# Kernel optimization log

Hardware: AMD Instinct MI355X
Metric: run time of the kernel (lower is better)

## Reference

```python
import jax, jax.numpy as jnp
import numpy as np
import math

NUM_PAGES = 256   # total KV pool pages
PAGE_SIZE = 16    # tokens per page
N_USED = 128      # pages in this sequence -> kv_len = 2048
H = 32            # num_heads
D = 128           # head_dim
LQ = 2048         # query length (== kv_len, causal prefill)


def setup_inputs() -> dict:
    key = jax.random.key(0)
    k_q, k_k, k_v, k_ks, k_vs = jax.random.split(key, 5)
    q = jax.random.normal(k_q, (1, H, LQ, D), dtype=jnp.float32)
    K_pages = jax.random.randint(k_k, (NUM_PAGES, PAGE_SIZE, H, D), -128, 128, dtype=jnp.int8)
    V_pages = jax.random.randint(k_v, (NUM_PAGES, PAGE_SIZE, H, D), -128, 128, dtype=jnp.int8)
    K_scale = jax.random.uniform(k_ks, (NUM_PAGES, 1, H, 1), dtype=jnp.float16, minval=0.001, maxval=0.02)
    V_scale = jax.random.uniform(k_vs, (NUM_PAGES, 1, H, 1), dtype=jnp.float16, minval=0.001, maxval=0.02)
    pages = jnp.arange(N_USED, dtype=jnp.int32)  # page table for this sequence
    return {"q": q, "K_pages": K_pages, "V_pages": V_pages,
            "K_scale": K_scale, "V_scale": V_scale, "pages": pages}


def _gather_dequant(pages_i8, scales, page_ids):
    # pages_i8: [P, ps, H, D] int8; scales: [P, 1, H, 1] fp16; page_ids: [n]
    x = pages_i8[page_ids].astype(jnp.float32) * scales[page_ids].astype(jnp.float32)
    n, ps, h, d = x.shape
    # cat along tokens, then [S,H,D] -> [1,H,S,D]
    return jnp.transpose(x.reshape(n * ps, h, d), (1, 0, 2))[None]


def reference(q, K_pages, V_pages, K_scale, V_scale, pages):
    K = _gather_dequant(K_pages, K_scale, pages)  # [1,H,S,D]
    V = _gather_dequant(V_pages, V_scale, pages)  # [1,H,S,D]
    lq = q.shape[2]
    s = K.shape[2]
    scale = 1.0 / math.sqrt(q.shape[-1])
    scores = jnp.einsum('bhqd,bhkd->bhqk', q, K) * scale  # [1,H,LQ,S]
    # torch is_causal: top-left aligned causal mask (j <= i)
    causal = jnp.tril(jnp.ones((lq, s), dtype=bool))
    scores = jnp.where(causal[None, None], scores, -jnp.inf)
    attn = jax.nn.softmax(scores, axis=-1)
    return jnp.einsum('bhqk,bhkd->bhqd', attn, V)
```

## Files before the change

### kernel.cpp

```cpp
#include <hip/hip_runtime.h>
#include <stdint.h>

#define NHEADS 32
#define DHEAD  128
#define LQ     2048
#define PAGE   16
#define QTILE  64
#define NQT    32
#define KVB    32
#define KPAD   136

typedef _Float16 f16x8 __attribute__((ext_vector_type(8)));
typedef _Float16 f16x2v __attribute__((ext_vector_type(2)));
typedef float    f32x4 __attribute__((ext_vector_type(4)));

__global__ __launch_bounds__(256, 2)
void paged_attn_kernel(const float* __restrict__ q,
                       const int*   __restrict__ Kp,
                       const int*   __restrict__ Vp,
                       const float* __restrict__ Kscale,
                       const float* __restrict__ Vscale,
                       const int*   __restrict__ pages,
                       float* __restrict__ out)
{
    __shared__ _Float16 Ks[KVB][KPAD];
    __shared__ __align__(16) _Float16 Vt[DHEAD][KVB];

    const int tid  = threadIdx.x;
    const int w    = tid >> 6;
    const int lane = tid & 63;
    const int g    = lane >> 4;
    const int c    = lane & 15;

    const int bx = blockIdx.x;
    const int h  = bx & (NHEADS - 1);
    const int p  = bx >> 5;
    const int qa = p, qb = NQT - 1 - p;
    const int q0a = qa * QTILE, q0b = qb * QTILE;

    const float qscale = 0.08838834764831845f * 1.44269504088896340736f;

    f16x8 qfa[4], qfb[4];
    {
        const float* qpa = q + ((size_t)h * LQ + q0a + w * 16 + c) * DHEAD;
        const float* qpb = q + ((size_t)h * LQ + q0b + w * 16 + c) * DHEAD;
        #pragma unroll
        for (int t = 0; t < 4; ++t)
            #pragma unroll
            for (int i = 0; i < 8; ++i) {
                qfa[t][i] = (_Float16)(qpa[t * 32 + g * 8 + i] * qscale);
                qfb[t][i] = (_Float16)(qpb[t * 32 + g * 8 + i] * qscale);
            }
    }

    f32x4 oaccA[8], oaccB[8];
    #pragma unroll
    for (int d = 0; d < 8; ++d) { oaccA[d] = (f32x4){0,0,0,0}; oaccB[d] = (f32x4){0,0,0,0}; }
    float mA = -1e30f, lA = 0.f, mB = -1e30f, lB = 0.f;

    const int ntiles = 2 * qb + 2;
    const int skv = tid >> 3;
    const int sa  = tid & 7;
    char* vtb = (char*)&Vt[0][0];

    auto issue = [&](int tile, int4* krD, int4* vrD, float& ksD, float& vsD) {
        const int t_glob = tile * KVB + skv;
        const int pg  = pages[t_glob >> 4];
        const int tok = t_glob & 15;
        const size_t base = (((size_t)pg * PAGE + tok) * NHEADS + h) * DHEAD + sa * 16;
        const int4* kp4 = (const int4*)(Kp + base);
        const int4* vp4 = (const int4*)(Vp + base);
        #pragma unroll
        for (int j = 0; j < 4; ++j) { krD[j] = kp4[j]; vrD[j] = vp4[j]; }
        ksD = Kscale[pg * NHEADS + h];
        vsD = Vscale[pg * NHEADS + h];
    };

    auto compute = [&](int kv0, const f16x8 (*kf)[4], const f16x8* qf, int q0t,
                       f32x4* oacc, float& mr, float& lr) {
        f32x4 s0 = (f32x4){0,0,0,0}, s1 = (f32x4){0,0,0,0};
        #pragma unroll
        for (int t = 0; t < 4; ++t) {
            s0 = __builtin_amdgcn_mfma_f32_16x16x32_f16(kf[0][t], qf[t], s0, 0, 0, 0);
            s1 = __builtin_amdgcn_mfma_f32_16x16x32_f16(kf[1][t], qf[t], s1, 0, 0, 0);
        }
        const int dq = (q0t + w * 16 + c) - (kv0 + 4 * g);
        #pragma unroll
        for (int r = 0; r < 4; ++r) {
            if (r > dq)      s0[r] = -1e30f;
            if (r > dq - 16) s1[r] = -1e30f;
        }
        float tm = fmaxf(fmaxf(fmaxf(s0[0], s0[1]), fmaxf(s0[2], s0[3])),
                         fmaxf(fmaxf(s1[0], s1[1]), fmaxf(s1[2], s1[3])));
        tm = fmaxf(tm, __shfl_xor(tm, 16, 64));
        tm = fmaxf(tm, __shfl_xor(tm, 32, 64));
        const float mn    = fmaxf(mr, tm);
        const float alpha = exp2f(mr - mn);
        mr = mn;
        float p0[4], p1[4];
        #pragma unroll
        for (int r = 0; r < 4; ++r) {
            p0[r] = exp2f(s0[r] - mn);
            p1[r] = exp2f(s1[r] - mn);
        }
        float rs = ((p0[0] + p0[1]) + (p0[2] + p0[3])) +
                   ((p1[0] + p1[1]) + (p1[2] + p1[3]));
        rs += __shfl_xor(rs, 16, 64);
        rs += __shfl_xor(rs, 32, 64);
        lr = lr * alpha + rs;
        float aR[4];
        #pragma unroll
        for (int r = 0; r < 4; ++r) aR[r] = __shfl(alpha, 20 * g + r, 64);
        #pragma unroll
        for (int d = 0; d < 8; ++d)
            #pragma unroll
            for (int r = 0; r < 4; ++r)
                oacc[d][r] *= aR[r];
        f16x2v t0, t1, t2, t3;
        t0[0] = (_Float16)p0[0]; t0[1] = (_Float16)p0[1];
        t1[0] = (_Float16)p0[2]; t1[1] = (_Float16)p0[3];
        t2[0] = (_Float16)p1[0]; t2[1] = (_Float16)p1[1];
        t3[0] = (_Float16)p1[2]; t3[1] = (_Float16)p1[3];
        const int w00 = __builtin_bit_cast(int, t0);
        const int w01 = __builtin_bit_cast(int, t1);
        const int w10 = __builtin_bit_cast(int, t2);
        const int w11 = __builtin_bit_cast(int, t3);
        const int srcL = ((g & 1) << 5) | c;
        const int srcH = srcL + 16;
        const int e0A = __shfl(w00, srcL, 64), e0B = __shfl(w10, srcL, 64);
        const int e1A = __shfl(w01, srcL, 64), e1B = __shfl(w11, srcL, 64);
        const int e2A = __shfl(w00, srcH, 64), e2B = __shfl(w10, srcH, 64);
        const int e3A = __shfl(w01, srcH, 64), e3B = __shfl(w11, srcH, 64);
        const bool hi = g >= 2;
        uint4 aw;
        aw.x = (unsigned)(hi ? e0B : e0A);
        aw.y = (unsigned)(hi ? e1B : e1A);
        aw.z = (unsigned)(hi ? e2B : e2A);
        aw.w = (unsigned)(hi ? e3B : e3A);
        const f16x8 pa = __builtin_bit_cast(f16x8, aw);
        #pragma unroll
        for (int d = 0; d < 8; ++d) {
            const int dcol = d * 16 + c;
            unsigned off = (unsigned)(dcol * (KVB * 2) + g * 16);
            off ^= (unsigned)(((dcol >> 3) & 7) << 4);
            f16x8 vf = *(const f16x8*)(vtb + off);
            oacc[d] = __builtin_amdgcn_mfma_f32_16x16x32_f16(pa, vf, oacc[d], 0, 0, 0);
        }
    };

    int4 krA[4], vrA[4]; float ksrA = 0.f, vsrA = 0.f;
    int4 krB[4], vrB[4]; float ksrB = 0.f, vsrB = 0.f;
    issue(0, krA, vrA, ksrA, vsrA);

    for (int tile = 0; tile < ntiles; ++tile) {
        const int kv0 = tile * KVB;

        {
            const int* ki = (const int*)krA;
            const int* vi = (const int*)vrA;
            f16x8 klo, khi;
            #pragma unroll
            for (int i = 0; i < 8; ++i) {
                klo[i] = (_Float16)((float)ki[i]     * ksrA);
                khi[i] = (_Float16)((float)ki[8 + i] * ksrA);
            }
            *(f16x8*)&Ks[skv][sa * 16]     = klo;
            *(f16x8*)&Ks[skv][sa * 16 + 8] = khi;
            #pragma unroll
            for (int j = 0; j < 16; ++j) {
                const int dcol = sa * 16 + j;
                unsigned off = (unsigned)(dcol * (KVB * 2) + skv * 2);
                off ^= (unsigned)(((dcol >> 3) & 7) << 4);
                *(_Float16*)(vtb + off) = (_Float16)((float)vi[j] * vsrA);
            }
        }
        __syncthreads();

        if (tile + 1 < ntiles) issue(tile + 1, krB, vrB, ksrB, vsrB);

        f16x8 kf[2][4];
        #pragma unroll
        for (int t = 0; t < 4; ++t) {
            kf[0][t] = *(const f16x8*)&Ks[c][t * 32 + g * 8];
            kf[1][t] = *(const f16x8*)&Ks[16 + c][t * 32 + g * 8];
        }

        if (kv0 <= q0b + w * 16 + 15)
            compute(kv0, kf, qfb, q0b, oaccB, mB, lB);
        if (kv0 <= q0a + w * 16 + 15)
            compute(kv0, kf, qfa, q0a, oaccA, mA, lA);

        __syncthreads();

        if (tile + 1 < ntiles) {
            #pragma unroll
            for (int j = 0; j < 4; ++j) { krA[j] = krB[j]; vrA[j] = vrB[j]; }
            ksrA = ksrB; vsrA = vsrB;
        }
    }

    float iA[4], iB[4];
    #pragma unroll
    for (int r = 0; r < 4; ++r) {
        iA[r] = 1.f / __shfl(lA, 20 * g + r, 64);
        iB[r] = 1.f / __shfl(lB, 20 * g + r, 64);
    }
    const int qgA = q0a + w * 16 + g * 4;
    const int qgB = q0b + w * 16 + g * 4;
    #pragma unroll
    for (int d = 0; d < 8; ++d)
        #pragma unroll
        for (int r = 0; r < 4; ++r) {
            out[((size_t)h * LQ + qgA + r) * DHEAD + d * 16 + c] = oaccA[d][r] * iA[r];
            out[((size_t)h * LQ + qgB + r) * DHEAD + d * 16 + c] = oaccB[d][r] * iB[r];
        }
}

extern "C" void kernel_launch(void* const* d_in, const int* in_sizes, int n_in,
                              void* d_out, int out_size, void* d_ws, size_t ws_size,
                              hipStream_t stream) {
    (void)in_sizes; (void)n_in; (void)d_ws; (void)ws_size; (void)out_size;
    const float* qp = (const float*)d_in[0];
    const int*   kp = (const int*)d_in[1];
    const int*   vp = (const int*)d_in[2];
    const float* ks = (const float*)d_in[3];
    const float* vs = (const float*)d_in[4];
    const int*   pg = (const int*)d_in[5];
    float*       op = (float*)d_out;

    dim3 grid(NHEADS * (NQT / 2));
    dim3 block(256);
    paged_attn_kernel<<<grid, block, 0, stream>>>(qp, kp, vp, ks, vs, pg, op);
}
```

Measured before the change: 265.3 us.

## Double-buffer LDS K/V tiles to drop one barrier per iteration

```diff
diff --git a/kernel.cpp b/kernel.cpp
--- a/kernel.cpp
+++ b/kernel.cpp
@@ -23,8 +23,8 @@
                        const int*   __restrict__ pages,
                        float* __restrict__ out)
 {
-    __shared__ _Float16 Ks[KVB][KPAD];
-    __shared__ __align__(16) _Float16 Vt[DHEAD][KVB];
+    __shared__ _Float16 Ks[2][KVB][KPAD];
+    __shared__ __align__(16) _Float16 Vt[2][DHEAD][KVB];
 
     const int tid  = threadIdx.x;
     const int w    = tid >> 6;
@@ -61,7 +61,6 @@
     const int ntiles = 2 * qb + 2;
     const int skv = tid >> 3;
     const int sa  = tid & 7;
-    char* vtb = (char*)&Vt[0][0];
 
     auto issue = [&](int tile, int4* krD, int4* vrD, float& ksD, float& vsD) {
         const int t_glob = tile * KVB + skv;
@@ -76,8 +75,29 @@
         vsD = Vscale[pg * NHEADS + h];
     };
 
-    auto compute = [&](int kv0, const f16x8 (*kf)[4], const f16x8* qf, int q0t,
-                       f32x4* oacc, float& mr, float& lr) {
+    auto stage = [&](int b, const int4* kr4, const int4* vr4, float ksr, float vsr) {
+        const int* ki = (const int*)kr4;
+        const int* vi = (const int*)vr4;
+        f16x8 klo, khi;
+        #pragma unroll
+        for (int i = 0; i < 8; ++i) {
+            klo[i] = (_Float16)((float)ki[i]     * ksr);
+            khi[i] = (_Float16)((float)ki[8 + i] * ksr);
+        }
+        *(f16x8*)&Ks[b][skv][sa * 16]     = klo;
+        *(f16x8*)&Ks[b][skv][sa * 16 + 8] = khi;
+        char* vtb = (char*)&Vt[b][0][0];
+        #pragma unroll
+        for (int j = 0; j < 16; ++j) {
+            const int dcol = sa * 16 + j;
+            unsigned off = (unsigned)(dcol * (KVB * 2) + skv * 2);
+            off ^= (unsigned)(((dcol >> 3) & 7) << 4);
+            *(_Float16*)(vtb + off) = (_Float16)((float)vi[j] * vsr);
+        }
+    };
+
+    auto compute = [&](int kv0, const f16x8 (*kf)[4], const f16x8* vf,
+                       const f16x8* qf, int q0t, f32x4* oacc, float& mr, float& lr) {
         f32x4 s0 = (f32x4){0,0,0,0}, s1 = (f32x4){0,0,0,0};
         #pragma unroll
         for (int t = 0; t < 4; ++t) {
@@ -139,64 +159,45 @@
         aw.w = (unsigned)(hi ? e3B : e3A);
         const f16x8 pa = __builtin_bit_cast(f16x8, aw);
         #pragma unroll
+        for (int d = 0; d < 8; ++d)
+            oacc[d] = __builtin_amdgcn_mfma_f32_16x16x32_f16(pa, vf[d], oacc[d], 0, 0, 0);
+    };
+
+    int4 krB[4], vrB[4]; float ksrB = 0.f, vsrB = 0.f;
+    issue(0, krB, vrB, ksrB, vsrB);
+    stage(0, krB, vrB, ksrB, vsrB);
+    if (ntiles > 1) issue(1, krB, vrB, ksrB, vsrB);
+    __syncthreads();
+
+    for (int t = 0; t < ntiles; ++t) {
+        const int b   = t & 1;
+        const int kv0 = t * KVB;
+
+        f16x8 kf[2][4], vf[8];
+        #pragma unroll
+        for (int tt = 0; tt < 4; ++tt) {
+            kf[0][tt] = *(const f16x8*)&Ks[b][c][tt * 32 + g * 8];
+            kf[1][tt] = *(const f16x8*)&Ks[b][16 + c][tt * 32 + g * 8];
+        }
+        const char* vtb = (const char*)&Vt[b][0][0];
+        #pragma unroll
         for (int d = 0; d < 8; ++d) {
             const int dcol = d * 16 + c;
             unsigned off = (unsigned)(dcol * (KVB * 2) + g * 16);
             off ^= (unsigned)(((dcol >> 3) & 7) << 4);
-            f16x8 vf = *(const f16x8*)(vtb + off);
-            oacc[d] = __builtin_amdgcn_mfma_f32_16x16x32_f16(pa, vf, oacc[d], 0, 0, 0);
-        }
-    };
-
-    int4 krA[4], vrA[4]; float ksrA = 0.f, vsrA = 0.f;
-    int4 krB[4], vrB[4]; float ksrB = 0.f, vsrB = 0.f;
-    issue(0, krA, vrA, ksrA, vsrA);
-
-    for (int tile = 0; tile < ntiles; ++tile) {
-        const int kv0 = tile * KVB;
-
-        {
-            const int* ki = (const int*)krA;
-            const int* vi = (const int*)vrA;
-            f16x8 klo, khi;
-            #pragma unroll
-            for (int i = 0; i < 8; ++i) {
-                klo[i] = (_Float16)((float)ki[i]     * ksrA);
-                khi[i] = (_Float16)((float)ki[8 + i] * ksrA);
-            }
-            *(f16x8*)&Ks[skv][sa * 16]     = klo;
-            *(f16x8*)&Ks[skv][sa * 16 + 8] = khi;
-            #pragma unroll
-            for (int j = 0; j < 16; ++j) {
-                const int dcol = sa * 16 + j;
-                unsigned off = (unsigned)(dcol * (KVB * 2) + skv * 2);
-                off ^= (unsigned)(((dcol >> 3) & 7) << 4);
-                *(_Float16*)(vtb + off) = (_Float16)((float)vi[j] * vsrA);
-            }
+            vf[d] = *(const f16x8*)(vtb + off);
+        }
+
+        if (kv0 <= q0b + w * 16 + 15)
+            compute(kv0, kf, vf, qfb, q0b, oaccB, mB, lB);
+        if (kv0 <= q0a + w * 16 + 15)
+            compute(kv0, kf, vf, qfa, q0a, oaccA, mA, lA);
+
+        if (t + 1 < ntiles) {
+            stage((t + 1) & 1, krB, vrB, ksrB, vsrB);
+            if (t + 2 < ntiles) issue(t + 2, krB, vrB, ksrB, vsrB);
         }
         __syncthreads();
-
-        if (tile + 1 < ntiles) issue(tile + 1, krB, vrB, ksrB, vsrB);
-
-        f16x8 kf[2][4];
-        #pragma unroll
-        for (int t = 0; t < 4; ++t) {
-            kf[0][t] = *(const f16x8*)&Ks[c][t * 32 + g * 8];
-            kf[1][t] = *(const f16x8*)&Ks[16 + c][t * 32 + g * 8];
-        }
-
-        if (kv0 <= q0b + w * 16 + 15)
-            compute(kv0, kf, qfb, q0b, oaccB, mB, lB);
-        if (kv0 <= q0a + w * 16 + 15)
-            compute(kv0, kf, qfa, q0a, oaccA, mA, lA);
-
-        __syncthreads();
-
-        if (tile + 1 < ntiles) {
-            #pragma unroll
-            for (int j = 0; j < 4; ++j) { krA[j] = krB[j]; vrA[j] = vrB[j]; }
-            ksrA = ksrB; vsrA = vsrB;
-        }
     }
 
     float iA[4], iB[4];
```

Result: slower. 277.8 us (+4.7%).

## Double KV tile to 64 rows, pack V transpose stores, skip rescale when max unchanged

Applied to the files above, without the earlier changes.

```diff
diff --git a/kernel.cpp b/kernel.cpp
--- a/kernel.cpp
+++ b/kernel.cpp
@@ -7,7 +7,7 @@
 #define PAGE   16
 #define QTILE  64
 #define NQT    32
-#define KVB    32
+#define KVB    64
 #define KPAD   136
 
 typedef _Float16 f16x8 __attribute__((ext_vector_type(8)));
@@ -24,7 +24,7 @@
                        float* __restrict__ out)
 {
     __shared__ _Float16 Ks[KVB][KPAD];
-    __shared__ __align__(16) _Float16 Vt[DHEAD][KVB];
+    __shared__ __align__(16) _Float16 Vt[2][DHEAD][32];
 
     const int tid  = threadIdx.x;
     const int w    = tid >> 6;
@@ -58,145 +58,174 @@
     for (int d = 0; d < 8; ++d) { oaccA[d] = (f32x4){0,0,0,0}; oaccB[d] = (f32x4){0,0,0,0}; }
     float mA = -1e30f, lA = 0.f, mB = -1e30f, lB = 0.f;
 
-    const int ntiles = 2 * qb + 2;
+    const int ntiles = qb + 1;
     const int skv = tid >> 3;
     const int sa  = tid & 7;
-    char* vtb = (char*)&Vt[0][0];
-
-    auto issue = [&](int tile, int4* krD, int4* vrD, float& ksD, float& vsD) {
-        const int t_glob = tile * KVB + skv;
-        const int pg  = pages[t_glob >> 4];
-        const int tok = t_glob & 15;
-        const size_t base = (((size_t)pg * PAGE + tok) * NHEADS + h) * DHEAD + sa * 16;
-        const int4* kp4 = (const int4*)(Kp + base);
-        const int4* vp4 = (const int4*)(Vp + base);
-        #pragma unroll
-        for (int j = 0; j < 4; ++j) { krD[j] = kp4[j]; vrD[j] = vp4[j]; }
-        ksD = Kscale[pg * NHEADS + h];
-        vsD = Vscale[pg * NHEADS + h];
+    const int tp  = tid >> 4;
+    const int do8 = (tid & 15) * 8;
+
+    int4 kr[8], vr[8];
+    float ksc2[2], vsc2[2];
+
+    auto issue = [&](int t) {
+        #pragma unroll
+        for (int hh = 0; hh < 2; ++hh) {
+            const int rowk = t * KVB + hh * 32 + skv;
+            const int pgk  = pages[rowk >> 4];
+            const size_t bk = (((size_t)pgk * PAGE + (rowk & 15)) * NHEADS + h) * DHEAD + sa * 16;
+            const int4* kp4 = (const int4*)(Kp + bk);
+            #pragma unroll
+            for (int j = 0; j < 4; ++j) kr[hh * 4 + j] = kp4[j];
+            ksc2[hh] = Kscale[pgk * NHEADS + h];
+
+            const int rowv = t * KVB + hh * 32 + 2 * tp;
+            const int pgv  = pages[rowv >> 4];
+            const size_t bv = (((size_t)pgv * PAGE + (rowv & 15)) * NHEADS + h) * DHEAD + do8;
+            const int4* vp4  = (const int4*)(Vp + bv);
+            const int4* vp4b = (const int4*)(Vp + bv + (size_t)NHEADS * DHEAD);
+            vr[hh * 4 + 0] = vp4[0];  vr[hh * 4 + 1] = vp4[1];
+            vr[hh * 4 + 2] = vp4b[0]; vr[hh * 4 + 3] = vp4b[1];
+            vsc2[hh] = Vscale[pgv * NHEADS + h];
+        }
     };
 
-    auto compute = [&](int kv0, const f16x8 (*kf)[4], const f16x8* qf, int q0t,
+    auto stage = [&]() {
+        #pragma unroll
+        for (int hh = 0; hh < 2; ++hh) {
+            const int* ki = (const int*)&kr[hh * 4];
+            const float ks = ksc2[hh];
+            f16x8 klo, khi;
+            #pragma unroll
+            for (int i = 0; i < 8; ++i) {
+                klo[i] = (_Float16)((float)ki[i]     * ks);
+                khi[i] = (_Float16)((float)ki[8 + i] * ks);
+            }
+            *(f16x8*)&Ks[hh * 32 + skv][sa * 16]     = klo;
+            *(f16x8*)&Ks[hh * 32 + skv][sa * 16 + 8] = khi;
+
+            const int* vi = (const int*)&vr[hh * 4];
+            const float vs = vsc2[hh];
+            char* vtb = (char*)&Vt[hh][0][0];
+            #pragma unroll
+            for (int j = 0; j < 8; ++j) {
+                const int dcol = do8 + j;
+                f16x2v pv;
+                pv[0] = (_Float16)((float)vi[j]     * vs);
+                pv[1] = (_Float16)((float)vi[8 + j] * vs);
+                unsigned off = (unsigned)(dcol * 64 + tp * 4);
+                off ^= (unsigned)(((dcol >> 3) & 7) << 4);
+                *(int*)(vtb + off) = __builtin_bit_cast(int, pv);
+            }
+        }
+    };
+
+    auto compute = [&](int kv0, const f16x8* qf, int q0t,
                        f32x4* oacc, float& mr, float& lr) {
-        f32x4 s0 = (f32x4){0,0,0,0}, s1 = (f32x4){0,0,0,0};
-        #pragma unroll
-        for (int t = 0; t < 4; ++t) {
-            s0 = __builtin_amdgcn_mfma_f32_16x16x32_f16(kf[0][t], qf[t], s0, 0, 0, 0);
-            s1 = __builtin_amdgcn_mfma_f32_16x16x32_f16(kf[1][t], qf[t], s1, 0, 0, 0);
+        f32x4 s[4];
+        #pragma unroll
+        for (int idx = 0; idx < 4; ++idx) {
+            s[idx] = (f32x4){0, 0, 0, 0};
+            #pragma unroll
+            for (int t = 0; t < 4; ++t) {
+                f16x8 kf = *(const f16x8*)&Ks[idx * 16 + c][t * 32 + g * 8];
+                s[idx] = __builtin_amdgcn_mfma_f32_16x16x32_f16(kf, qf[t], s[idx], 0, 0, 0);
+            }
         }
         const int dq = (q0t + w * 16 + c) - (kv0 + 4 * g);
         #pragma unroll
-        for (int r = 0; r < 4; ++r) {
-            if (r > dq)      s0[r] = -1e30f;
-            if (r > dq - 16) s1[r] = -1e30f;
-        }
-        float tm = fmaxf(fmaxf(fmaxf(s0[0], s0[1]), fmaxf(s0[2], s0[3])),
-                         fmaxf(fmaxf(s1[0], s1[1]), fmaxf(s1[2], s1[3])));
+        for (int idx = 0; idx < 4; ++idx)
+            #pragma unroll
+            for (int r = 0; r < 4; ++r)
+                if (r > dq - 16 * idx) s[idx][r] = -1e30f;
+        float tm = -1e30f;
+        #pragma unroll
+        for (int idx = 0; idx < 4; ++idx)
+            #pragma unroll
+            for (int r = 0; r < 4; ++r) tm = fmaxf(tm, s[idx][r]);
         tm = fmaxf(tm, __shfl_xor(tm, 16, 64));
         tm = fmaxf(tm, __shfl_xor(tm, 32, 64));
-        const float mn    = fmaxf(mr, tm);
-        const float alpha = exp2f(mr - mn);
-        mr = mn;
-        float p0[4], p1[4];
-        #pragma unroll
-        for (int r = 0; r < 4; ++r) {
-            p0[r] = exp2f(s0[r] - mn);
-            p1[r] = exp2f(s1[r] - mn);
-        }
-        float rs = ((p0[0] + p0[1]) + (p0[2] + p0[3])) +
-                   ((p1[0] + p1[1]) + (p1[2] + p1[3]));
+
+        const bool fast = __all(tm <= mr);
+        float mn = mr;
+        float alpha = 1.f;
+        if (!fast) {
+            mn = fmaxf(mr, tm);
+            alpha = exp2f(mr - mn);
+            mr = mn;
+        }
+        float rs = 0.f;
+        #pragma unroll
+        for (int idx = 0; idx < 4; ++idx)
+            #pragma unroll
+            for (int r = 0; r < 4; ++r) {
+                s[idx][r] = exp2f(s[idx][r] - mn);
+                rs += s[idx][r];
+            }
         rs += __shfl_xor(rs, 16, 64);
         rs += __shfl_xor(rs, 32, 64);
-        lr = lr * alpha + rs;
-        float aR[4];
-        #pragma unroll
-        for (int r = 0; r < 4; ++r) aR[r] = __shfl(alpha, 20 * g + r, 64);
-        #pragma unroll
-        for (int d = 0; d < 8; ++d)
-            #pragma unroll
-            for (int r = 0; r < 4; ++r)
-                oacc[d][r] *= aR[r];
-        f16x2v t0, t1, t2, t3;
-        t0[0] = (_Float16)p0[0]; t0[1] = (_Float16)p0[1];
-        t1[0] = (_Float16)p0[2]; t1[1] = (_Float16)p0[3];
-        t2[0] = (_Float16)p1[0]; t2[1] = (_Float16)p1[1];
-        t3[0] = (_Float16)p1[2]; t3[1] = (_Float16)p1[3];
-        const int w00 = __builtin_bit_cast(int, t0);
-        const int w01 = __builtin_bit_cast(int, t1);
-        const int w10 = __builtin_bit_cast(int, t2);
-        const int w11 = __builtin_bit_cast(int, t3);
-        const int srcL = ((g & 1) << 5) | c;
-        const int srcH = srcL + 16;
-        const int e0A = __shfl(w00, srcL, 64), e0B = __shfl(w10, srcL, 64);
-        const int e1A = __shfl(w01, srcL, 64), e1B = __shfl(w11, srcL, 64);
-        const int e2A = __shfl(w00, srcH, 64), e2B = __shfl(w10, srcH, 64);
-        const int e3A = __shfl(w01, srcH, 64), e3B = __shfl(w11, srcH, 64);
-        const bool hi = g >= 2;
-        uint4 aw;
-        aw.x = (unsigned)(hi ? e0B : e0A);
-        aw.y = (unsigned)(hi ? e1B : e1A);
-        aw.z = (unsigned)(hi ? e2B : e2A);
-        aw.w = (unsigned)(hi ? e3B : e3A);
-        const f16x8 pa = __builtin_bit_cast(f16x8, aw);
+        if (fast) {
+            lr += rs;
+        } else {
+            lr = lr * alpha + rs;
+            float aR[4];
+            #pragma unroll
+            for (int r = 0; r < 4; ++r) aR[r] = __shfl(alpha, 20 * g + r, 64);
+            #pragma unroll
+            for (int d = 0; d < 8; ++d)
+                #pragma unroll
+                for (int r = 0; r < 4; ++r)
+                    oacc[d][r] *= aR[r];
+        }
+        f16x8 pa[2];
+        #pragma unroll
+        for (int hh = 0; hh < 2; ++hh) {
+            f16x2v t0, t1, t2, t3;
+            t0[0] = (_Float16)s[2*hh][0];   t0[1] = (_Float16)s[2*hh][1];
+            t1[0] = (_Float16)s[2*hh][2];   t1[1] = (_Float16)s[2*hh][3];
+            t2[0] = (_Float16)s[2*hh+1][0]; t2[1] = (_Float16)s[2*hh+1][1];
+            t3[0] = (_Float16)s[2*hh+1][2]; t3[1] = (_Float16)s[2*hh+1][3];
+            const int w00 = __builtin_bit_cast(int, t0);
+            const int w01 = __builtin_bit_cast(int, t1);
+            const int w10 = __builtin_bit_cast(int, t2);
+            const int w11 = __builtin_bit_cast(int, t3);
+            const int srcL = ((g & 1) << 5) | c;
+            const int srcH = srcL + 16;
+            const int e0A = __shfl(w00, srcL, 64), e0B = __shfl(w10, srcL, 64);
+            const int e1A = __shfl(w01, srcL, 64), e1B = __shfl(w11, srcL, 64);
+            const int e2A = __shfl(w00, srcH, 64), e2B = __shfl(w10, srcH, 64);
+            const int e3A = __shfl(w01, srcH, 64), e3B = __shfl(w11, srcH, 64);
+            const bool hi = g >= 2;
+            uint4 aw;
+            aw.x = (unsigned)(hi ? e0B : e0A);
+            aw.y = (unsigned)(hi ? e1B : e1A);
+            aw.z = (unsigned)(hi ? e2B : e2A);
+            aw.w = (unsigned)(hi ? e3B : e3A);
+            pa[hh] = __builtin_bit_cast(f16x8, aw);
+        }
         #pragma unroll
         for (int d = 0; d < 8; ++d) {
             const int dcol = d * 16 + c;
-            unsigned off = (unsigned)(dcol * (KVB * 2) + g * 16);
+            unsigned off = (unsigned)(dcol * 64 + g * 16);
             off ^= (unsigned)(((dcol >> 3) & 7) << 4);
-            f16x8 vf = *(const f16x8*)(vtb + off);
-            oacc[d] = __builtin_amdgcn_mfma_f32_16x16x32_f16(pa, vf, oacc[d], 0, 0, 0);
+            f16x8 vfL = *(const f16x8*)((const char*)&Vt[0][0][0] + off);
+            f16x8 vfH = *(const f16x8*)((const char*)&Vt[1][0][0] + off);
+            oacc[d] = __builtin_amdgcn_mfma_f32_16x16x32_f16(pa[0], vfL, oacc[d], 0, 0, 0);
+            oacc[d] = __builtin_amdgcn_mfma_f32_16x16x32_f16(pa[1], vfH, oacc[d], 0, 0, 0);
         }
     };
 
-    int4 krA[4], vrA[4]; float ksrA = 0.f, vsrA = 0.f;
-    int4 krB[4], vrB[4]; float ksrB = 0.f, vsrB = 0.f;
-    issue(0, krA, vrA, ksrA, vsrA);
-
-    for (int tile = 0; tile < ntiles; ++tile) {
-        const int kv0 = tile * KVB;
-
-        {
-            const int* ki = (const int*)krA;
-            const int* vi = (const int*)vrA;
-            f16x8 klo, khi;
-            #pragma unroll
-            for (int i = 0; i < 8; ++i) {
-                klo[i] = (_Float16)((float)ki[i]     * ksrA);
-                khi[i] = (_Float16)((float)ki[8 + i] * ksrA);
-            }
-            *(f16x8*)&Ks[skv][sa * 16]     = klo;
-            *(f16x8*)&Ks[skv][sa * 16 + 8] = khi;
-            #pragma unroll
-            for (int j = 0; j < 16; ++j) {
-                const int dcol = sa * 16 + j;
-                unsigned off = (unsigned)(dcol * (KVB * 2) + skv * 2);
-                off ^= (unsigned)(((dcol >> 3) & 7) << 4);
-                *(_Float16*)(vtb + off) = (_Float16)((float)vi[j] * vsrA);
-            }
-        }
+    issue(0);
+    for (int t = 0; t < ntiles; ++t) {
+        const int kv0 = t * KVB;
+        stage();
         __syncthreads();
-
-        if (tile + 1 < ntiles) issue(tile + 1, krB, vrB, ksrB, vsrB);
-
-        f16x8 kf[2][4];
-        #pragma unroll
-        for (int t = 0; t < 4; ++t) {
-            kf[0][t] = *(const f16x8*)&Ks[c][t * 32 + g * 8];
-            kf[1][t] = *(const f16x8*)&Ks[16 + c][t * 32 + g * 8];
-        }
-
-        if (kv0 <= q0b + w * 16 + 15)
-            compute(kv0, kf, qfb, q0b, oaccB, mB, lB);
+        if (t + 1 < ntiles) issue(t + 1);
+
+        compute(kv0, qfb, q0b, oaccB, mB, lB);
         if (kv0 <= q0a + w * 16 + 15)
-            compute(kv0, kf, qfa, q0a, oaccA, mA, lA);
+            compute(kv0, qfa, q0a, oaccA, mA, lA);
 
         __syncthreads();
-
-        if (tile + 1 < ntiles) {
-            #pragma unroll
-            for (int j = 0; j < 4; ++j) { krA[j] = krB[j]; vrA[j] = vrB[j]; }
-            ksrA = ksrB; vsrA = vsrB;
-        }
     }
 
     float iA[4], iB[4];
```

Result: slower. 398.6 us (+50.2%).

## Pack V staging writes, skip rescale when max is unchanged, prioritise MFMA

Applied to the files above, without the earlier changes.

```diff
diff --git a/kernel.cpp b/kernel.cpp
--- a/kernel.cpp
+++ b/kernel.cpp
@@ -61,29 +61,68 @@
     const int ntiles = 2 * qb + 2;
     const int skv = tid >> 3;
     const int sa  = tid & 7;
-    char* vtb = (char*)&Vt[0][0];
-
-    auto issue = [&](int tile, int4* krD, int4* vrD, float& ksD, float& vsD) {
-        const int t_glob = tile * KVB + skv;
-        const int pg  = pages[t_glob >> 4];
-        const int tok = t_glob & 15;
-        const size_t base = (((size_t)pg * PAGE + tok) * NHEADS + h) * DHEAD + sa * 16;
-        const int4* kp4 = (const int4*)(Kp + base);
-        const int4* vp4 = (const int4*)(Vp + base);
-        #pragma unroll
-        for (int j = 0; j < 4; ++j) { krD[j] = kp4[j]; vrD[j] = vp4[j]; }
-        ksD = Kscale[pg * NHEADS + h];
-        vsD = Vscale[pg * NHEADS + h];
+    const int tp  = tid >> 4;
+    const int do8 = (tid & 15) * 8;
+
+    int4 kr[4], vr[4];
+    float ksr = 0.f, vsr = 0.f;
+
+    auto issue = [&](int t) {
+        const int rowk = t * KVB + skv;
+        const int pgk  = pages[rowk >> 4];
+        const size_t bk = (((size_t)pgk * PAGE + (rowk & 15)) * NHEADS + h) * DHEAD + sa * 16;
+        const int4* kp4 = (const int4*)(Kp + bk);
+        #pragma unroll
+        for (int j = 0; j < 4; ++j) kr[j] = kp4[j];
+        ksr = Kscale[pgk * NHEADS + h];
+
+        const int rowv = t * KVB + 2 * tp;
+        const int pgv  = pages[rowv >> 4];
+        const size_t bv = (((size_t)pgv * PAGE + (rowv & 15)) * NHEADS + h) * DHEAD + do8;
+        const int4* vp4  = (const int4*)(Vp + bv);
+        const int4* vp4b = (const int4*)(Vp + bv + (size_t)NHEADS * DHEAD);
+        vr[0] = vp4[0];  vr[1] = vp4[1];
+        vr[2] = vp4b[0]; vr[3] = vp4b[1];
+        vsr = Vscale[pgv * NHEADS + h];
     };
 
-    auto compute = [&](int kv0, const f16x8 (*kf)[4], const f16x8* qf, int q0t,
+    auto stage = [&]() {
+        const int* ki = (const int*)kr;
+        f16x8 klo, khi;
+        #pragma unroll
+        for (int i = 0; i < 8; ++i) {
+            klo[i] = (_Float16)((float)ki[i]     * ksr);
+            khi[i] = (_Float16)((float)ki[8 + i] * ksr);
+        }
+        *(f16x8*)&Ks[skv][sa * 16]     = klo;
+        *(f16x8*)&Ks[skv][sa * 16 + 8] = khi;
+
+        const int* vi = (const int*)vr;
+        char* vtb = (char*)&Vt[0][0];
+        #pragma unroll
+        for (int j = 0; j < 8; ++j) {
+            const int dcol = do8 + j;
+            f16x2v pv;
+            pv[0] = (_Float16)((float)vi[j]     * vsr);
+            pv[1] = (_Float16)((float)vi[8 + j] * vsr);
+            unsigned off = (unsigned)(dcol * (KVB * 2) + tp * 4);
+            off ^= (unsigned)(((dcol >> 3) & 7) << 4);
+            *(int*)(vtb + off) = __builtin_bit_cast(int, pv);
+        }
+    };
+
+    auto compute = [&](int kv0, const f16x8* qf, int q0t,
                        f32x4* oacc, float& mr, float& lr) {
         f32x4 s0 = (f32x4){0,0,0,0}, s1 = (f32x4){0,0,0,0};
+        __builtin_amdgcn_s_setprio(1);
         #pragma unroll
         for (int t = 0; t < 4; ++t) {
-            s0 = __builtin_amdgcn_mfma_f32_16x16x32_f16(kf[0][t], qf[t], s0, 0, 0, 0);
-            s1 = __builtin_amdgcn_mfma_f32_16x16x32_f16(kf[1][t], qf[t], s1, 0, 0, 0);
-        }
+            f16x8 kf0 = *(const f16x8*)&Ks[c][t * 32 + g * 8];
+            f16x8 kf1 = *(const f16x8*)&Ks[16 + c][t * 32 + g * 8];
+            s0 = __builtin_amdgcn_mfma_f32_16x16x32_f16(kf0, qf[t], s0, 0, 0, 0);
+            s1 = __builtin_amdgcn_mfma_f32_16x16x32_f16(kf1, qf[t], s1, 0, 0, 0);
+        }
+        __builtin_amdgcn_s_setprio(0);
         const int dq = (q0t + w * 16 + c) - (kv0 + 4 * g);
         #pragma unroll
         for (int r = 0; r < 4; ++r) {
@@ -94,28 +133,34 @@
                          fmaxf(fmaxf(s1[0], s1[1]), fmaxf(s1[2], s1[3])));
         tm = fmaxf(tm, __shfl_xor(tm, 16, 64));
         tm = fmaxf(tm, __shfl_xor(tm, 32, 64));
-        const float mn    = fmaxf(mr, tm);
-        const float alpha = exp2f(mr - mn);
-        mr = mn;
+
+        const bool fast = __all(tm <= mr);
+        float mn = mr;
+        if (!fast) {
+            mn = fmaxf(mr, tm);
+            const float alpha = exp2f(mr - mn);
+            mr = mn;
+            float aR[4];
+            #pragma unroll
+            for (int r = 0; r < 4; ++r) aR[r] = __shfl(alpha, 20 * g + r, 64);
+            lr *= alpha;
+            #pragma unroll
+            for (int d = 0; d < 8; ++d)
+                #pragma unroll
+                for (int r = 0; r < 4; ++r)
+                    oacc[d][r] *= aR[r];
+        }
         float p0[4], p1[4];
+        float rs = 0.f;
         #pragma unroll
         for (int r = 0; r < 4; ++r) {
             p0[r] = exp2f(s0[r] - mn);
             p1[r] = exp2f(s1[r] - mn);
-        }
-        float rs = ((p0[0] + p0[1]) + (p0[2] + p0[3])) +
-                   ((p1[0] + p1[1]) + (p1[2] + p1[3]));
+            rs += p0[r] + p1[r];
+        }
         rs += __shfl_xor(rs, 16, 64);
         rs += __shfl_xor(rs, 32, 64);
-        lr = lr * alpha + rs;
-        float aR[4];
-        #pragma unroll
-        for (int r = 0; r < 4; ++r) aR[r] = __shfl(alpha, 20 * g + r, 64);
-        #pragma unroll
-        for (int d = 0; d < 8; ++d)
-            #pragma unroll
-            for (int r = 0; r < 4; ++r)
-                oacc[d][r] *= aR[r];
+        lr += rs;
         f16x2v t0, t1, t2, t3;
         t0[0] = (_Float16)p0[0]; t0[1] = (_Float16)p0[1];
         t1[0] = (_Float16)p0[2]; t1[1] = (_Float16)p0[3];
@@ -138,65 +183,30 @@
         aw.z = (unsigned)(hi ? e2B : e2A);
         aw.w = (unsigned)(hi ? e3B : e3A);
         const f16x8 pa = __builtin_bit_cast(f16x8, aw);
+        __builtin_amdgcn_s_setprio(1);
         #pragma unroll
         for (int d = 0; d < 8; ++d) {
             const int dcol = d * 16 + c;
             unsigned off = (unsigned)(dcol * (KVB * 2) + g * 16);
             off ^= (unsigned)(((dcol >> 3) & 7) << 4);
-            f16x8 vf = *(const f16x8*)(vtb + off);
+            f16x8 vf = *(const f16x8*)((const char*)&Vt[0][0] + off);
             oacc[d] = __builtin_amdgcn_mfma_f32_16x16x32_f16(pa, vf, oacc[d], 0, 0, 0);
         }
+        __builtin_amdgcn_s_setprio(0);
     };
 
-    int4 krA[4], vrA[4]; float ksrA = 0.f, vsrA = 0.f;
-    int4 krB[4], vrB[4]; float ksrB = 0.f, vsrB = 0.f;
-    issue(0, krA, vrA, ksrA, vsrA);
-
-    for (int tile = 0; tile < ntiles; ++tile) {
-        const int kv0 = tile * KVB;
-
-        {
-            const int* ki = (const int*)krA;
-            const int* vi = (const int*)vrA;
-            f16x8 klo, khi;
-            #pragma unroll
-            for (int i = 0; i < 8; ++i) {
-                klo[i] = (_Float16)((float)ki[i]     * ksrA);
-                khi[i] = (_Float16)((float)ki[8 + i] * ksrA);
-            }
-            *(f16x8*)&Ks[skv][sa * 16]     = klo;
-            *(f16x8*)&Ks[skv][sa * 16 + 8] = khi;
-            #pragma unroll
-            for (int j = 0; j < 16; ++j) {
-                const int dcol = sa * 16 + j;
-                unsigned off = (unsigned)(dcol * (KVB * 2) + skv * 2);
-                off ^= (unsigned)(((dcol >> 3) & 7) << 4);
-                *(_Float16*)(vtb + off) = (_Float16)((float)vi[j] * vsrA);
-            }
-        }
+    issue(0);
+    for (int t = 0; t < ntiles; ++t) {
+        const int kv0 = t * KVB;
+        stage();
         __syncthreads();
-
-        if (tile + 1 < ntiles) issue(tile + 1, krB, vrB, ksrB, vsrB);
-
-        f16x8 kf[2][4];
-        #pragma unroll
-        for (int t = 0; t < 4; ++t) {
-            kf[0][t] = *(const f16x8*)&Ks[c][t * 32 + g * 8];
-            kf[1][t] = *(const f16x8*)&Ks[16 + c][t * 32 + g * 8];
-        }
-
-        if (kv0 <= q0b + w * 16 + 15)
-            compute(kv0, kf, qfb, q0b, oaccB, mB, lB);
+        if (t + 1 < ntiles) issue(t + 1);
+
+        compute(kv0, qfb, q0b, oaccB, mB, lB);
         if (kv0 <= q0a + w * 16 + 15)
-            compute(kv0, kf, qfa, q0a, oaccA, mA, lA);
+            compute(kv0, qfa, q0a, oaccA, mA, lA);
 
         __syncthreads();
-
-        if (tile + 1 < ntiles) {
-            #pragma unroll
-            for (int j = 0; j < 4; ++j) { krA[j] = krB[j]; vrA[j] = vrB[j]; }
-            ksrA = ksrB; vsrA = vsrB;
-        }
     }
 
     float iA[4], iB[4];
```

Measured after the change: 259.1 us. 1.02x faster.
